# Kernel optimization log

Hardware: AMD Instinct MI355X
Metric: run time of the kernel (lower is better)

## Reference

```python
import jax, jax.numpy as jnp
import numpy as np

N = 8192
IN_F = 256
OUT_F = 256
ATTN_DIM = 2
NEG_INF = -1e18


def setup_inputs() -> dict:
    key = jax.random.key(0)
    k1, k2, k3, k4, k5 = jax.random.split(key, 5)
    node_feats = jax.random.normal(k1, (N, IN_F), dtype=jnp.float32)
    Ahat = (jax.random.uniform(k2, (N, N)) < 0.01).astype(jnp.float32)
    # ensure no isolated rows (self loops) so softmax rows are well-defined
    Ahat = Ahat.at[jnp.arange(N), jnp.arange(N)].set(1.0)
    bound_w = 1.0 / np.sqrt(IN_F)
    bound_wa = 1.0 / np.sqrt(OUT_F)
    bound_a = 1.0 / np.sqrt(2 * ATTN_DIM)
    w = jax.random.uniform(k3, (IN_F, OUT_F), minval=-bound_w, maxval=bound_w, dtype=jnp.float32)
    w_a = jax.random.uniform(k4, (OUT_F, ATTN_DIM), minval=-bound_wa, maxval=bound_wa, dtype=jnp.float32)
    a = jax.random.uniform(k5, (2 * ATTN_DIM, 1), minval=-bound_a, maxval=bound_a, dtype=jnp.float32)
    return {"node_feats": node_feats, "Ahat": Ahat, "w": w, "w_a": w_a, "a": a}


def reference(node_feats, Ahat, w, w_a, a):
    # h_prime: [N, out_features]
    h_prime = node_feats @ w
    # h_reduced: [N, attn_dim]
    h_reduced = h_prime @ w_a
    # e[i, j] = cat(h_red[i], h_red[j]) @ a  ==  h_red[i]@a[:d] + h_red[j]@a[d:]
    # (identical math to the repeat+cat+matmul in the original, without the
    #  O(N^2 * 2d) materialization)
    f_src = (h_reduced @ a[:ATTN_DIM]).squeeze(-1)  # [N]
    f_dst = (h_reduced @ a[ATTN_DIM:]).squeeze(-1)  # [N]
    e = f_src[:, None] + f_dst[None, :]             # [N, N]
    masked_e = jnp.where(Ahat > 0, e, NEG_INF)
    attn_scores = jax.nn.softmax(masked_e, axis=-1)  # [N, N]
    out = attn_scores @ h_prime                      # [N, out_features]
    return jax.nn.relu(out)
```

## Files before the change

kernel.cpp:

```cpp
#include <hip/hip_runtime.h>
#include <hip/hip_bf16.h>
#include <math.h>

#define NN 8192
#define IN_F 256
#define OUT_F 256

typedef _Float16 half4_t __attribute__((ext_vector_type(4)));
typedef float    f4_t    __attribute__((ext_vector_type(4)));
typedef short    short8  __attribute__((ext_vector_type(8)));
typedef float    f32x4   __attribute__((ext_vector_type(4)));
typedef unsigned short us8 __attribute__((ext_vector_type(8)));

__global__ __launch_bounds__(256) void prep_wt_frag(
    const float* __restrict__ W,
    unsigned short* __restrict__ WtHi,
    unsigned short* __restrict__ WtLo)
{
    const int fid  = blockIdx.x * 256 + threadIdx.x;
    const int lane = fid & 63;
    const int kb   = (fid >> 6) & 7;
    const int cb   = fid >> 9;
    const int c    = cb * 16 + (lane & 15);
    const int k    = kb * 32 + (lane >> 4) * 8;

    us8 hi, lo;
#pragma unroll
    for (int e = 0; e < 8; ++e) {
        const float x = W[(size_t)(k + e) * OUT_F + c];
        const unsigned int bx = __float_as_uint(x);
        const unsigned int hb = bx & 0xFFFF0000u;
        hi[e] = (unsigned short)(hb >> 16);
        const float lf = x - __uint_as_float(hb);
        lo[e] = (unsigned short)(__float_as_uint(lf) >> 16);
    }
    ((us8*)WtHi)[fid] = hi;
    ((us8*)WtLo)[fid] = lo;
}

__device__ __forceinline__ void split8(const float4 a, const float4 b,
                                       short8& hi, short8& lo) {
    const float x[8] = {a.x, a.y, a.z, a.w, b.x, b.y, b.z, b.w};
#pragma unroll
    for (int i = 0; i < 8; ++i) {
        const unsigned int bx = __float_as_uint(x[i]);
        const unsigned int hb = bx & 0xFFFF0000u;
        hi[i] = (short)(hb >> 16);
        const float lf = x[i] - __uint_as_float(hb);
        lo[i] = (short)(__float_as_uint(lf) >> 16);
    }
}

__global__ __launch_bounds__(256) void gemm_hprime_mfma(
    const float* __restrict__ X,
    const unsigned short* __restrict__ WtHi,
    const unsigned short* __restrict__ WtLo,
    _Float16* __restrict__ H16)
{
    const int w    = threadIdx.x >> 6;
    const int lane = threadIdx.x & 63;
    const int c0   = blockIdx.x * 64;
    const int cb0  = blockIdx.x * 4;
    const int rw0  = blockIdx.y * 64 + w * 16;

    const int ar = lane & 15;
    const int ko = lane >> 4;

    const short8* BH = (const short8*)WtHi;
    const short8* BL = (const short8*)WtLo;

    f32x4 acc[4] = {};

    const float* xrow = X + (size_t)(rw0 + ar) * IN_F + ko * 8;

#pragma unroll
    for (int kb = 0; kb < 8; ++kb) {
        const float4 xa = *(const float4*)(xrow + kb * 32);
        const float4 xb = *(const float4*)(xrow + kb * 32 + 4);
        short8 ahi, alo;
        split8(xa, xb, ahi, alo);

#pragma unroll
        for (int nc = 0; nc < 4; ++nc) {
            const int fid = ((cb0 + nc) * 8 + kb) * 64 + lane;
            const short8 bhi = BH[fid];
            const short8 blo = BL[fid];
            acc[nc] = __builtin_amdgcn_mfma_f32_16x16x32_bf16(ahi, bhi, acc[nc], 0, 0, 0);
            acc[nc] = __builtin_amdgcn_mfma_f32_16x16x32_bf16(ahi, blo, acc[nc], 0, 0, 0);
            acc[nc] = __builtin_amdgcn_mfma_f32_16x16x32_bf16(alo, bhi, acc[nc], 0, 0, 0);
        }
    }

    const int orow = rw0 + (lane >> 4) * 4;
    const int ocol = c0 + (lane & 15);
#pragma unroll
    for (int nc = 0; nc < 4; ++nc)
#pragma unroll
        for (int i = 0; i < 4; ++i)
            H16[(size_t)(orow + i) * OUT_F + ocol + nc * 16] = (_Float16)acc[nc][i];
}

__global__ __launch_bounds__(256) void fdst_exp(
    const _Float16* __restrict__ hp16,
    const float* __restrict__ w_a,
    const float* __restrict__ a,
    float* __restrict__ fexp)
{
    const int row  = blockIdx.x * 4 + (threadIdx.x >> 6);
    const int lane = threadIdx.x & 63;

    const float a2 = a[2];
    const float a3 = a[3];

    const half4_t h  = ((const half4_t*)hp16)[(size_t)row * 64 + lane];
    const float4 wa0 = *(const float4*)(w_a + lane * 8);
    const float4 wa1 = *(const float4*)(w_a + lane * 8 + 4);

    float s = (float)h.x * fmaf(wa0.x, a2, wa0.y * a3)
            + (float)h.y * fmaf(wa0.z, a2, wa0.w * a3)
            + (float)h.z * fmaf(wa1.x, a2, wa1.y * a3)
            + (float)h.w * fmaf(wa1.z, a2, wa1.w * a3);

#pragma unroll
    for (int off = 32; off > 0; off >>= 1) s += __shfl_xor(s, off, 64);

    if (lane == 0) fexp[row] = expf(s);
}

#define CAPW 192

__global__ __launch_bounds__(256) void attn_aggregate(
    const float* __restrict__ Ahat,
    const _Float16* __restrict__ hp16,
    const float* __restrict__ fexp,
    float* __restrict__ out)
{
    __shared__ int s_idx[4 * CAPW];

    const int wid  = threadIdx.x >> 6;
    const int lane = threadIdx.x & 63;
    const int row  = blockIdx.x * 4 + wid;
    int* const my_idx = s_idx + wid * CAPW;

    const f4_t* arow   = (const f4_t*)(Ahat + (size_t)row * NN);
    const half4_t* hp4 = (const half4_t*)hp16;

    float4 acc = {0.0f, 0.0f, 0.0f, 0.0f};
    float den = 0.0f;
    int cnt = 0;
    int kproc = 0;

#define BATCH8(kk)                                                            \
    {                                                                         \
        const int4 ja = *(const int4*)(my_idx + (kk));                        \
        const int4 jb = *(const int4*)(my_idx + (kk) + 4);                    \
        const float p0 = fexp[ja.x], p1 = fexp[ja.y], p2 = fexp[ja.z], p3 = fexp[ja.w]; \
        const float p4 = fexp[jb.x], p5 = fexp[jb.y], p6 = fexp[jb.z], p7 = fexp[jb.w]; \
        const half4_t h0 = hp4[((size_t)ja.x << 6) + lane];                   \
        const half4_t h1 = hp4[((size_t)ja.y << 6) + lane];                   \
        const half4_t h2 = hp4[((size_t)ja.z << 6) + lane];                   \
        const half4_t h3 = hp4[((size_t)ja.w << 6) + lane];                   \
        const half4_t h4 = hp4[((size_t)jb.x << 6) + lane];                   \
        const half4_t h5 = hp4[((size_t)jb.y << 6) + lane];                   \
        const half4_t h6 = hp4[((size_t)jb.z << 6) + lane];                   \
        const half4_t h7 = hp4[((size_t)jb.w << 6) + lane];                   \
        acc.x = fmaf(p0, (float)h0.x, acc.x); acc.y = fmaf(p0, (float)h0.y, acc.y); \
        acc.z = fmaf(p0, (float)h0.z, acc.z); acc.w = fmaf(p0, (float)h0.w, acc.w); \
        acc.x = fmaf(p1, (float)h1.x, acc.x); acc.y = fmaf(p1, (float)h1.y, acc.y); \
        acc.z = fmaf(p1, (float)h1.z, acc.z); acc.w = fmaf(p1, (float)h1.w, acc.w); \
        acc.x = fmaf(p2, (float)h2.x, acc.x); acc.y = fmaf(p2, (float)h2.y, acc.y); \
        acc.z = fmaf(p2, (float)h2.z, acc.z); acc.w = fmaf(p2, (float)h2.w, acc.w); \
        acc.x = fmaf(p3, (float)h3.x, acc.x); acc.y = fmaf(p3, (float)h3.y, acc.y); \
        acc.z = fmaf(p3, (float)h3.z, acc.z); acc.w = fmaf(p3, (float)h3.w, acc.w); \
        acc.x = fmaf(p4, (float)h4.x, acc.x); acc.y = fmaf(p4, (float)h4.y, acc.y); \
        acc.z = fmaf(p4, (float)h4.z, acc.z); acc.w = fmaf(p4, (float)h4.w, acc.w); \
        acc.x = fmaf(p5, (float)h5.x, acc.x); acc.y = fmaf(p5, (float)h5.y, acc.y); \
        acc.z = fmaf(p5, (float)h5.z, acc.z); acc.w = fmaf(p5, (float)h5.w, acc.w); \
        acc.x = fmaf(p6, (float)h6.x, acc.x); acc.y = fmaf(p6, (float)h6.y, acc.y); \
        acc.z = fmaf(p6, (float)h6.z, acc.z); acc.w = fmaf(p6, (float)h6.w, acc.w); \
        acc.x = fmaf(p7, (float)h7.x, acc.x); acc.y = fmaf(p7, (float)h7.y, acc.y); \
        acc.z = fmaf(p7, (float)h7.z, acc.z); acc.w = fmaf(p7, (float)h7.w, acc.w); \
        den += ((p0 + p1) + (p2 + p3)) + ((p4 + p5) + (p6 + p7));              \
    }

    f4_t v0 = __builtin_nontemporal_load(arow + lane);
    f4_t v1 = __builtin_nontemporal_load(arow + 64 + lane);

    for (int c = 0; c < 32; ++c) {
        const f4_t cur = v0;
        v0 = v1;
        if (c + 2 < 32) v1 = __builtin_nontemporal_load(arow + (c + 2) * 64 + lane);

        const int jbase = c * 256 + lane * 4;

#define COMPACT(pred, comp)                                                   \
        {                                                                     \
            const unsigned long long m = __ballot(pred);                      \
            const unsigned int lo = __builtin_amdgcn_mbcnt_lo((unsigned)m, 0);\
            const int pos = cnt + (int)__builtin_amdgcn_mbcnt_hi(             \
                                        (unsigned)(m >> 32), lo);             \
            if ((pred) && pos < CAPW) my_idx[pos] = jbase + (comp);           \
            cnt += __builtin_popcountll(m);                                   \
        }

        COMPACT(cur.x > 0.0f, 0)
        COMPACT(cur.y > 0.0f, 1)
        COMPACT(cur.z > 0.0f, 2)
        COMPACT(cur.w > 0.0f, 3)
#undef COMPACT

        const int lim = cnt < CAPW ? cnt : CAPW;
        while (kproc + 8 <= lim) {
            BATCH8(kproc);
            kproc += 8;
        }
    }
#undef BATCH8

    const int lim = cnt < CAPW ? cnt : CAPW;
    for (; kproc < lim; ++kproc) {
        const int j = my_idx[kproc];
        const float p = fexp[j];
        const half4_t h = hp4[((size_t)j << 6) + lane];
        acc.x = fmaf(p, (float)h.x, acc.x);
        acc.y = fmaf(p, (float)h.y, acc.y);
        acc.z = fmaf(p, (float)h.z, acc.z);
        acc.w = fmaf(p, (float)h.w, acc.w);
        den += p;
    }

    const float inv = 1.0f / den;
    float4 o;
    o.x = fmaxf(acc.x * inv, 0.0f);
    o.y = fmaxf(acc.y * inv, 0.0f);
    o.z = fmaxf(acc.z * inv, 0.0f);
    o.w = fmaxf(acc.w * inv, 0.0f);
    *(float4*)(out + (size_t)row * OUT_F + lane * 4) = o;
}

extern "C" void kernel_launch(void* const* d_in, const int* in_sizes, int n_in,
                              void* d_out, int out_size, void* d_ws, size_t ws_size,
                              hipStream_t stream) {
    const float* node_feats = (const float*)d_in[0];
    const float* Ahat       = (const float*)d_in[1];
    const float* w          = (const float*)d_in[2];
    const float* w_a        = (const float*)d_in[3];
    const float* a          = (const float*)d_in[4];
    float* out = (float*)d_out;

    _Float16* hp16 = (_Float16*)d_ws;
    float* fexp = (float*)((char*)d_ws + (size_t)NN * OUT_F * 2);
    unsigned short* WtHi = (unsigned short*)((char*)fexp + NN * 4);
    unsigned short* WtLo = WtHi + IN_F * OUT_F;

    prep_wt_frag<<<32, 256, 0, stream>>>(w, WtHi, WtLo);
    gemm_hprime_mfma<<<dim3(OUT_F / 64, NN / 64), 256, 0, stream>>>(node_feats, WtHi, WtLo, hp16);
    fdst_exp<<<dim3(NN / 4), 256, 0, stream>>>(hp16, w_a, a, fexp);
    attn_aggregate<<<dim3(NN / 4), 256, 0, stream>>>(Ahat, hp16, fexp, out);
}
```

Before: 397.4 us.

## Software-pipeline rows per wave: gather previous row while scanning next Ahat row

Each wave now handles four consecutive rows. It compacts the neighbour indices of the current row into a double-buffered LDS list while spreading the gather-FMA batches of the previous row evenly across the scan chunks. Ahat prefetch depth goes from two to three chunks. The aim is to overlap the streaming read of the 256MB adjacency with the random gathers of h_prime and reduce latency stalls. In exchange the grid shrinks by four, so fewer waves are in flight, and register pressure rises.

```diff
diff --git a/kernel.cpp b/kernel.cpp
--- a/kernel.cpp
+++ b/kernel.cpp
@@ -128,6 +128,7 @@
 }
 
 #define CAPW 192
+#define RPW 4
 
 __global__ __launch_bounds__(256) void attn_aggregate(
     const float* __restrict__ Ahat,
@@ -135,25 +136,18 @@
     const float* __restrict__ fexp,
     float* __restrict__ out)
 {
-    __shared__ int s_idx[4 * CAPW];
-
-    const int wid  = threadIdx.x >> 6;
-    const int lane = threadIdx.x & 63;
-    const int row  = blockIdx.x * 4 + wid;
-    int* const my_idx = s_idx + wid * CAPW;
-
-    const f4_t* arow   = (const f4_t*)(Ahat + (size_t)row * NN);
+    __shared__ int s_idx[4][2][CAPW];
+
+    const int wid   = threadIdx.x >> 6;
+    const int lane  = threadIdx.x & 63;
+    const int rbase = (blockIdx.x * 4 + wid) * RPW;
+
     const half4_t* hp4 = (const half4_t*)hp16;
 
-    float4 acc = {0.0f, 0.0f, 0.0f, 0.0f};
-    float den = 0.0f;
-    int cnt = 0;
-    int kproc = 0;
-
-#define BATCH8(kk)                                                            \
+#define BATCH8(IDXP)                                                          \
     {                                                                         \
-        const int4 ja = *(const int4*)(my_idx + (kk));                        \
-        const int4 jb = *(const int4*)(my_idx + (kk) + 4);                    \
+        const int4 ja = *(const int4*)(IDXP);                                 \
+        const int4 jb = *(const int4*)((IDXP) + 4);                           \
         const float p0 = fexp[ja.x], p1 = fexp[ja.y], p2 = fexp[ja.z], p3 = fexp[ja.w]; \
         const float p4 = fexp[jb.x], p5 = fexp[jb.y], p6 = fexp[jb.z], p7 = fexp[jb.w]; \
         const half4_t h0 = hp4[((size_t)ja.x << 6) + lane];                   \
@@ -183,59 +177,107 @@
         den += ((p0 + p1) + (p2 + p3)) + ((p4 + p5) + (p6 + p7));              \
     }
 
-    f4_t v0 = __builtin_nontemporal_load(arow + lane);
-    f4_t v1 = __builtin_nontemporal_load(arow + 64 + lane);
-
-    for (int c = 0; c < 32; ++c) {
-        const f4_t cur = v0;
-        v0 = v1;
-        if (c + 2 < 32) v1 = __builtin_nontemporal_load(arow + (c + 2) * 64 + lane);
-
-        const int jbase = c * 256 + lane * 4;
+    float4 acc = {0.0f, 0.0f, 0.0f, 0.0f};
+    float den  = 0.0f;
+    int   cntP = 0;
+
+    for (int q = 0; q < RPW; ++q) {
+        const int row = rbase + q;
+        int* const curL       = &s_idx[wid][q & 1][0];
+        const int* const prvL = &s_idx[wid][(q & 1) ^ 1][0];
+        const f4_t* arow = (const f4_t*)(Ahat + (size_t)row * NN);
+
+        const int nb = cntP >> 3;
+        int done = 0;
+
+        int cnt = 0;
+        f4_t v0 = __builtin_nontemporal_load(arow + lane);
+        f4_t v1 = __builtin_nontemporal_load(arow + 64 + lane);
+        f4_t v2 = __builtin_nontemporal_load(arow + 128 + lane);
+
+        for (int c = 0; c < 32; ++c) {
+            const f4_t cur = v0;
+            v0 = v1;
+            v1 = v2;
+            if (c + 3 < 32) v2 = __builtin_nontemporal_load(arow + (c + 3) * 64 + lane);
+
+            const int jbase = c * 256 + lane * 4;
 
 #define COMPACT(pred, comp)                                                   \
-        {                                                                     \
-            const unsigned long long m = __ballot(pred);                      \
-            const unsigned int lo = __builtin_amdgcn_mbcnt_lo((unsigned)m, 0);\
-            const int pos = cnt + (int)__builtin_amdgcn_mbcnt_hi(             \
-                                        (unsigned)(m >> 32), lo);             \
-            if ((pred) && pos < CAPW) my_idx[pos] = jbase + (comp);           \
-            cnt += __builtin_popcountll(m);                                   \
-        }
-
-        COMPACT(cur.x > 0.0f, 0)
-        COMPACT(cur.y > 0.0f, 1)
-        COMPACT(cur.z > 0.0f, 2)
-        COMPACT(cur.w > 0.0f, 3)
+            {                                                                 \
+                const unsigned long long m = __ballot(pred);                  \
+                const unsigned int lo = __builtin_amdgcn_mbcnt_lo((unsigned)m, 0);\
+                const int pos = cnt + (int)__builtin_amdgcn_mbcnt_hi(         \
+                                            (unsigned)(m >> 32), lo);         \
+                if ((pred) && pos < CAPW) curL[pos] = jbase + (comp);         \
+                cnt += __builtin_popcountll(m);                               \
+            }
+
+            COMPACT(cur.x > 0.0f, 0)
+            COMPACT(cur.y > 0.0f, 1)
+            COMPACT(cur.z > 0.0f, 2)
+            COMPACT(cur.w > 0.0f, 3)
 #undef COMPACT
 
-        const int lim = cnt < CAPW ? cnt : CAPW;
-        while (kproc + 8 <= lim) {
-            BATCH8(kproc);
-            kproc += 8;
-        }
+            const int target = (nb * (c + 1)) >> 5;
+            while (done < target) {
+                BATCH8(prvL + done * 8);
+                ++done;
+            }
+        }
+
+        while (done < nb) {
+            BATCH8(prvL + done * 8);
+            ++done;
+        }
+        for (int k = nb * 8; k < cntP; ++k) {
+            const int j = prvL[k];
+            const float p = fexp[j];
+            const half4_t h = hp4[((size_t)j << 6) + lane];
+            acc.x = fmaf(p, (float)h.x, acc.x);
+            acc.y = fmaf(p, (float)h.y, acc.y);
+            acc.z = fmaf(p, (float)h.z, acc.z);
+            acc.w = fmaf(p, (float)h.w, acc.w);
+            den += p;
+        }
+        if (q > 0) {
+            const float inv = 1.0f / den;
+            float4 o;
+            o.x = fmaxf(acc.x * inv, 0.0f);
+            o.y = fmaxf(acc.y * inv, 0.0f);
+            o.z = fmaxf(acc.z * inv, 0.0f);
+            o.w = fmaxf(acc.w * inv, 0.0f);
+            *(float4*)(out + (size_t)(row - 1) * OUT_F + lane * 4) = o;
+        }
+
+        acc = (float4){0.0f, 0.0f, 0.0f, 0.0f};
+        den = 0.0f;
+        cntP = cnt < CAPW ? cnt : CAPW;
+    }
+
+    {
+        const int* const prvL = &s_idx[wid][(RPW - 1) & 1][0];
+        const int nb = cntP >> 3;
+        for (int b = 0; b < nb; ++b) BATCH8(prvL + b * 8);
+        for (int k = nb * 8; k < cntP; ++k) {
+            const int j = prvL[k];
+            const float p = fexp[j];
+            const half4_t h = hp4[((size_t)j << 6) + lane];
+            acc.x = fmaf(p, (float)h.x, acc.x);
+            acc.y = fmaf(p, (float)h.y, acc.y);
+            acc.z = fmaf(p, (float)h.z, acc.z);
+            acc.w = fmaf(p, (float)h.w, acc.w);
+            den += p;
+        }
+        const float inv = 1.0f / den;
+        float4 o;
+        o.x = fmaxf(acc.x * inv, 0.0f);
+        o.y = fmaxf(acc.y * inv, 0.0f);
+        o.z = fmaxf(acc.z * inv, 0.0f);
+        o.w = fmaxf(acc.w * inv, 0.0f);
+        *(float4*)(out + (size_t)(rbase + RPW - 1) * OUT_F + lane * 4) = o;
     }
 #undef BATCH8
-
-    const int lim = cnt < CAPW ? cnt : CAPW;
-    for (; kproc < lim; ++kproc) {
-        const int j = my_idx[kproc];
-        const float p = fexp[j];
-        const half4_t h = hp4[((size_t)j << 6) + lane];
-        acc.x = fmaf(p, (float)h.x, acc.x);
-        acc.y = fmaf(p, (float)h.y, acc.y);
-        acc.z = fmaf(p, (float)h.z, acc.z);
-        acc.w = fmaf(p, (float)h.w, acc.w);
-        den += p;
-    }
-
-    const float inv = 1.0f / den;
-    float4 o;
-    o.x = fmaxf(acc.x * inv, 0.0f);
-    o.y = fmaxf(acc.y * inv, 0.0f);
-    o.z = fmaxf(acc.z * inv, 0.0f);
-    o.w = fmaxf(acc.w * inv, 0.0f);
-    *(float4*)(out + (size_t)row * OUT_F + lane * 4) = o;
 }
 
 extern "C" void kernel_launch(void* const* d_in, const int* in_sizes, int n_in,
@@ -256,5 +298,5 @@
     prep_wt_frag<<<32, 256, 0, stream>>>(w, WtHi, WtLo);
     gemm_hprime_mfma<<<dim3(OUT_F / 64, NN / 64), 256, 0, stream>>>(node_feats, WtHi, WtLo, hp16);
     fdst_exp<<<dim3(NN / 4), 256, 0, stream>>>(hp16, w_a, a, fexp);
-    attn_aggregate<<<dim3(NN / 4), 256, 0, stream>>>(Ahat, hp16, fexp, out);
-}
+    attn_aggregate<<<dim3(NN / (4 * RPW)), 256, 0, stream>>>(Ahat, hp16, fexp, out);
+}
```

Measured after the change: 413.9 us. +4.2%, slower.
